# Performance work log

Hardware: AMD Instinct MI355X
Metric: run time of the kernel (lower is better)

The kernel has to match this reference:

```python
import jax, jax.numpy as jnp
import numpy as np

T, N, C, D, S = 512, 32, 1296, 512, 30
NORM_SCALE = 32.0
NEGINF = -1e9


def setup_inputs() -> dict:
    key = jax.random.key(0)
    k1, k2, k3, k4, k5 = jax.random.split(key, 5)
    feats = jax.random.normal(k1, (T * N, D), dtype=jnp.float32)
    classifier_weight = jax.random.normal(k2, (D, C), dtype=jnp.float32)
    labeling = jax.random.randint(k3, (N, S), 1, C)  # targets cannot be blank(0)
    logit_lgts = (T - jax.random.randint(k4, (N,), 0, 32)).astype(jnp.int32)
    labeling_lgts = (S - jax.random.randint(k5, (N,), 0, 5)).astype(jnp.int32)
    return dict(feats=feats, classifier_weight=classifier_weight,
                labeling=labeling, logit_lgts=logit_lgts, labeling_lgts=labeling_lgts)


def _ctc_loss(log_probs, labels, in_lens, lab_lens):
    # log_probs: (T, N, C); labels: (N, S); blank = 0; reduction = 'sum'
    Tt, Nn, Cc = log_probs.shape
    Ss = labels.shape[1]
    L = 2 * Ss + 1
    # extended labeling: blank, l1, blank, l2, ..., blank  -> (N, L)
    ext = jnp.zeros((Nn, L), dtype=labels.dtype).at[:, 1::2].set(labels)
    # gather per-state log-probs: (T, N, L)
    lp_ext = jnp.take_along_axis(log_probs, jnp.broadcast_to(ext[None], (Tt, Nn, L)), axis=2)
    # skip transition s-2 -> s allowed iff s > 1 and ext[s] != ext[s-2]
    skip_ok = jnp.concatenate(
        [jnp.zeros((Nn, 2), dtype=bool), ext[:, 2:] != ext[:, :-2]], axis=1)
    alpha0 = (jnp.full((Nn, L), NEGINF, dtype=log_probs.dtype)
              .at[:, 0].set(lp_ext[0, :, 0])
              .at[:, 1].set(lp_ext[0, :, 1]))

    def step(alpha, inp):
        lp_t, t = inp  # lp_t: (N, L)
        a1 = alpha
        a2 = jnp.pad(alpha[:, :-1], ((0, 0), (1, 0)), constant_values=NEGINF)
        a3 = jnp.where(skip_ok,
                       jnp.pad(alpha[:, :-2], ((0, 0), (2, 0)), constant_values=NEGINF),
                       NEGINF)
        new = jax.nn.logsumexp(jnp.stack([a1, a2, a3], axis=0), axis=0) + lp_t
        # freeze alpha once t reaches a sample's input length
        alpha = jnp.where((t < in_lens)[:, None], new, alpha)
        return alpha, None

    alpha, _ = jax.lax.scan(step, alpha0, (lp_ext[1:], jnp.arange(1, Tt)))
    Ln = 2 * lab_lens + 1  # (N,)
    last = jnp.take_along_axis(alpha, (Ln - 1)[:, None], axis=1)[:, 0]
    last2 = jnp.take_along_axis(alpha, (Ln - 2)[:, None], axis=1)[:, 0]
    nll = -jnp.logaddexp(last, last2)
    return jnp.sum(nll)


def reference(feats, classifier_weight, labeling, logit_lgts, labeling_lgts):
    # RadialCTC: cosine logits with norm_scale, then CTC on log-softmax.
    w_n = classifier_weight / jnp.linalg.norm(classifier_weight, axis=0, keepdims=True)  # (D, C)
    f_n = feats / jnp.linalg.norm(feats, axis=1, keepdims=True)  # (T*N, D)
    logits = NORM_SCALE * (f_n @ w_n)  # (T*N, C)
    log_probs = jax.nn.log_softmax(logits.reshape(T, N, C), axis=-1)
    return _ctc_loss(log_probs, labeling, logit_lgts, labeling_lgts)
```

## Files before the change

### kernel.cpp

```cpp
#include <hip/hip_runtime.h>
#include <stdint.h>
#include <stddef.h>


typedef _Float16 f16;
typedef _Float16 f16x8 __attribute__((ext_vector_type(8)));
typedef float f32x4 __attribute__((ext_vector_type(4)));
typedef __attribute__((address_space(1))) void* as1_void_ptr;
typedef __attribute__((address_space(3))) void* as3_void_ptr;

#define TT 512
#define NN 32
#define CC 1296
#define DD 512
#define SS 30
#define CP 1408
#define LL 61
#define NORM_SCALE 32.0f
#define LOG2E 1.4426950408889634f
#define LN2   0.6931471805599453f

#define PREP_WBLK (CP / 16)
#define PREP_ZBLK 16
#define PREP_FBLK (TT * NN / 4)

#define GEMM_BLK ((TT * NN / 128) * (CP / 128))
#define MEGA_GC  NN
#define MEGA_BLK (MEGA_GC + GEMM_BLK)

__device__ __forceinline__ float fexp2(float x) { return __builtin_amdgcn_exp2f(x); }
__device__ __forceinline__ float flog2(float x) { return __builtin_amdgcn_logf(x); }

__device__ __forceinline__ double dpp_sr1_zero64(double x) {
    long long b = __double_as_longlong(x);
    int lo = (int)(b & 0xFFFFFFFFLL);
    int hi = (int)(b >> 32);
    int lo2 = __builtin_amdgcn_update_dpp(0, lo, 0x138, 0xF, 0xF, false);
    int hi2 = __builtin_amdgcn_update_dpp(0, hi, 0x138, 0xF, 0xF, false);
    return __longlong_as_double(((long long)hi2 << 32) |
                                (unsigned long long)(unsigned int)lo2);
}
__device__ __forceinline__ double dpp_sl1_zero64(double x) {
    long long b = __double_as_longlong(x);
    int lo = (int)(b & 0xFFFFFFFFLL);
    int hi = (int)(b >> 32);
    int lo2 = __builtin_amdgcn_update_dpp(0, lo, 0x130, 0xF, 0xF, false);
    int hi2 = __builtin_amdgcn_update_dpp(0, hi, 0x130, 0xF, 0xF, false);
    return __longlong_as_double(((long long)hi2 << 32) |
                                (unsigned long long)(unsigned int)lo2);
}
__device__ __forceinline__ float dpp_sl1_zero32(float x) {
    int r = __builtin_amdgcn_update_dpp(0, __float_as_int(x), 0x130, 0xF, 0xF, false);
    return __int_as_float(r);
}
template <int CTRL>
__device__ __forceinline__ int dpp_imax_level(int m) {
    int t = __builtin_amdgcn_update_dpp(0, m, CTRL, 0xF, 0xF, false);
    return m > t ? m : t;
}
__device__ __forceinline__ void renorm_d(double& x, int& Mi) {
    int h = (int)(__double_as_longlong(x) >> 32);
    h = dpp_imax_level<0x111>(h);
    h = dpp_imax_level<0x112>(h);
    h = dpp_imax_level<0x114>(h);
    h = dpp_imax_level<0x118>(h);
    int r0 = __builtin_amdgcn_readlane(h, 15);
    int r1 = __builtin_amdgcn_readlane(h, 31);
    int r2 = __builtin_amdgcn_readlane(h, 47);
    int r3 = __builtin_amdgcn_readlane(h, 63);
    int mx = max(max(r0, r1), max(r2, r3));
    int e11 = mx >> 20;
    double scale = __longlong_as_double((long long)(2046 - e11) << 52);
    x *= scale;
    Mi += e11 - 1023;
}

__global__ __launch_bounds__(256) void prep_kernel(const float* __restrict__ W,
                                                   const float* __restrict__ feats,
                                                   f16* __restrict__ wt,
                                                   f16* __restrict__ fn,
                                                   float* __restrict__ sumexp) {
    int bx = blockIdx.x, tid = threadIdx.x;
    if (bx < PREP_WBLK) {
        __shared__ float red[256];
        __shared__ float rqs[16];
        int c0 = bx * 16;
        int cl = tid & 15, dg = tid >> 4;
        int c = c0 + cl;
        float ss = 0.f;
        if (c < CC) {
            for (int d = dg; d < DD; d += 16) {
                float v = W[(size_t)d * CC + c];
                ss += v * v;
            }
        }
        red[tid] = ss;
        __syncthreads();
        if (tid < 16) {
            float s2 = 0.f;
            #pragma unroll
            for (int k = 0; k < 16; ++k) s2 += red[tid + 16 * k];
            rqs[tid] = rsqrtf(s2);
        }
        __syncthreads();
        int c_loc = tid >> 4, dl = tid & 15;
        int cc = c0 + c_loc;
        float rq = rqs[c_loc];
        #pragma unroll 4
        for (int it = 0; it < 32; ++it) {
            int d = dl + it * 16;
            float v = (cc < CC) ? W[(size_t)d * CC + cc] * rq : 0.f;
            wt[(size_t)cc * DD + d] = (f16)v;
        }
    } else if (bx < PREP_WBLK + PREP_ZBLK) {
        int zb = bx - PREP_WBLK;
        float4 z = {0.f, 0.f, 0.f, 0.f};
        ((float4*)sumexp)[zb * 256 + tid] = z;
    } else {
        int fb = bx - PREP_WBLK - PREP_ZBLK;
        int wv = (fb * 256 + tid) >> 6;
        int lane = tid & 63;
        const float4* src = (const float4*)(feats + (size_t)wv * DD) + lane * 2;
        float4 a = src[0], b = src[1];
        float ss = a.x*a.x + a.y*a.y + a.z*a.z + a.w*a.w
                 + b.x*b.x + b.y*b.y + b.z*b.z + b.w*b.w;
        #pragma unroll
        for (int off = 32; off; off >>= 1) ss += __shfl_xor(ss, off);
        float r = rsqrtf(ss);
        f16x8 o;
        o[0]=(f16)(a.x*r); o[1]=(f16)(a.y*r); o[2]=(f16)(a.z*r); o[3]=(f16)(a.w*r);
        o[4]=(f16)(b.x*r); o[5]=(f16)(b.y*r); o[6]=(f16)(b.z*r); o[7]=(f16)(b.w*r);
        *(f16x8*)(fn + (size_t)wv * DD + lane * 8) = o;
    }
}

template <int NT>
__device__ __forceinline__ void gather_chunk(const f16* __restrict__ pb0,
                                             const f16* __restrict__ pb1,
                                             const f16* __restrict__ A,
                                             float* __restrict__ lp_lab,
                                             int n, int c, int rbase, int lane) {
    int lm = lane & 15, hi = lane >> 4;
    const f16* pa0 = A + ((size_t)(c * 128 + rbase + lm) * NN + n) * DD + hi * 8;
    f32x4 acc[NT][2];
    #pragma unroll
    for (int i = 0; i < NT; ++i) {
        acc[i][0] = (f32x4){0.f, 0.f, 0.f, 0.f};
        acc[i][1] = (f32x4){0.f, 0.f, 0.f, 0.f};
    }
    for (int kb = 0; kb < 16; ++kb) {
        f16x8 bf0 = *(const f16x8*)(pb0 + kb * 32);
        f16x8 bf1 = *(const f16x8*)(pb1 + kb * 32);
        #pragma unroll
        for (int i = 0; i < NT; ++i) {
            f16x8 af = *(const f16x8*)(pa0 + (size_t)(i * 16) * NN * DD + kb * 32);
            acc[i][0] = __builtin_amdgcn_mfma_f32_16x16x32_f16(af, bf0, acc[i][0], 0, 0, 0);
            acc[i][1] = __builtin_amdgcn_mfma_f32_16x16x32_f16(af, bf1, acc[i][1], 0, 0, 0);
        }
    }
    #pragma unroll
    for (int i = 0; i < NT; ++i) {
        #pragma unroll
        for (int jn = 0; jn < 2; ++jn) {
            int jc = jn * 16 + lm;
            if (jc >= 31) continue;
            float4 o;
            o.x = acc[i][jn][0] * (NORM_SCALE * LOG2E);
            o.y = acc[i][jn][1] * (NORM_SCALE * LOG2E);
            o.z = acc[i][jn][2] * (NORM_SCALE * LOG2E);
            o.w = acc[i][jn][3] * (NORM_SCALE * LOG2E);
            *(float4*)&lp_lab[((size_t)n * 31 + jc) * TT
                              + c * 128 + rbase + i * 16 + hi * 4] = o;
        }
    }
}

__global__ __launch_bounds__(256) void mega_kernel(const f16* __restrict__ A,
                                                   const f16* __restrict__ B,
                                                   const int* __restrict__ labels,
                                                   const int* __restrict__ in_lens,
                                                   const int* __restrict__ lab_lens,
                                                   float* __restrict__ sumexp,
                                                   float* __restrict__ lp_lab,
                                                   double* __restrict__ part) {
    __shared__ __align__(16) f16 sm[8192];
    int bx = blockIdx.x;
    int tid = threadIdx.x;
    int w = tid >> 6, lane = tid & 63;
    int lm = lane & 15, hi = lane >> 4;
    int sw = (lm >> 1) & 3;

    if (bx >= MEGA_GC) {
        int j = bx - MEGA_GC;
        int x = j & 7, rr = j >> 3;
        int bm = x * 16 + (rr & 15);
        int bn = rr >> 4;
        int wm = w >> 1, wn = w & 1;
        f32x4 acc[4][4];
        f32x4 zero = {0.f, 0.f, 0.f, 0.f};
        #pragma unroll
        for (int i = 0; i < 4; ++i)
            #pragma unroll
            for (int jj = 0; jj < 4; ++jj) acc[i][jj] = zero;

        for (int kb = 0; kb < 16; ++kb) {
            #pragma unroll
            for (int p = 0; p < 2; ++p) {
                int s = p * 256 + tid;
                int row = s >> 2;
                int ch = (s & 3) ^ ((row >> 1) & 3);
                const f16* ga = A + (size_t)(bm * 128 + row) * DD + kb * 32 + ch * 8;
                const f16* gb = B + (size_t)(bn * 128 + row) * DD + kb * 32 + ch * 8;
                __builtin_amdgcn_global_load_lds((as1_void_ptr)ga,
                    (as3_void_ptr)&sm[(p * 256 + w * 64) * 8], 16, 0, 0);
                __builtin_amdgcn_global_load_lds((as1_void_ptr)gb,
                    (as3_void_ptr)&sm[4096 + (p * 256 + w * 64) * 8], 16, 0, 0);
            }
            __syncthreads();
            f16x8 af[4], bf[4];
            #pragma unroll
            for (int i = 0; i < 4; ++i)
                af[i] = *(const f16x8*)&sm[(wm * 64 + i * 16 + lm) * 32 + (hi ^ sw) * 8];
            #pragma unroll
            for (int jj = 0; jj < 4; ++jj)
                bf[jj] = *(const f16x8*)&sm[4096 + (wn * 64 + jj * 16 + lm) * 32 + (hi ^ sw) * 8];
            #pragma unroll
            for (int i = 0; i < 4; ++i)
                #pragma unroll
                for (int jj = 0; jj < 4; ++jj)
                    acc[i][jj] = __builtin_amdgcn_mfma_f32_16x16x32_f16(af[i], bf[jj], acc[i][jj], 0, 0, 0);
            __syncthreads();
        }
        #pragma unroll
        for (int i = 0; i < 4; ++i) {
            float rs[4] = {0.f, 0.f, 0.f, 0.f};
            #pragma unroll
            for (int jj = 0; jj < 4; ++jj) {
                int c = bn * 128 + wn * 64 + jj * 16 + lm;
                bool ok = (c < CC);
                #pragma unroll
                for (int r = 0; r < 4; ++r)
                    rs[r] += ok ? fexp2(acc[i][jj][r] * (NORM_SCALE * LOG2E)) : 0.f;
            }
            #pragma unroll
            for (int off = 1; off < 16; off <<= 1) {
                #pragma unroll
                for (int r = 0; r < 4; ++r) rs[r] += __shfl_xor(rs[r], off);
            }
            if (lm == 0) {
                int rowb = bm * 128 + wm * 64 + i * 16 + hi * 4;
                #pragma unroll
                for (int r = 0; r < 4; ++r) atomicAdd(&sumexp[rowb + r], rs[r]);
            }
        }
        return;
    }

    int n = bx;
    if (w >= 2) {
        __builtin_amdgcn_s_setprio(2);
        int cls0 = (lm == 0) ? 0 : labels[n * SS + lm - 1];
        int cls1 = (lm >= 15) ? 0 : labels[n * SS + lm + 15];
        const f16* pb0 = B + (size_t)cls0 * DD + hi * 8;
        const f16* pb1 = B + (size_t)cls1 * DD + hi * 8;
        int cA = (w == 2) ? 0 : 3;
        int cB = (w == 2) ? 1 : 2;
        gather_chunk<4>(pb0, pb1, A, lp_lab, n, cA, 0, lane);
        gather_chunk<4>(pb0, pb1, A, lp_lab, n, cA, 64, lane);
        __syncthreads();
        gather_chunk<4>(pb0, pb1, A, lp_lab, n, cB, 0, lane);
        gather_chunk<4>(pb0, pb1, A, lp_lab, n, cB, 64, lane);
        __builtin_amdgcn_s_setprio(0);
        __syncthreads();
        __syncthreads();
        return;
    }

    int s = lane;
    bool valid = s < LL;
    int ext = (valid && (s & 1)) ? labels[n * SS + (s >> 1)] : 0;
    int jmap = (valid && (s & 1)) ? ((s >> 1) + 1) : 0;
    int Tin = in_lens[n];
    const float* lpr = lp_lab + ((size_t)n * 31 + jmap) * TT;
    double* vb = (double*)sm;

    if (w == 0) {
        int ext2 = __shfl_up(ext, 2);
        double skipd = ((s >= 2) && valid && (ext != ext2)) ? 1.0 : 0.0;
        double sk1 = dpp_sr1_zero64(skipd);
        double sk2 = dpp_sr1_zero64(sk1);
        double kk2 = skipd * sk2;
        const float4* g4 = (const float4*)lpr;
        double beta = 0.0;
        int Mif = 0;

        auto stepL = [&](float lp) {
            double P = (double)fexp2(lp);
            double b1 = dpp_sr1_zero64(beta);
            double b2 = dpp_sr1_zero64(b1);
            beta = (beta + b1 + b2 * skipd) * P;
        };
        auto step2 = [&](float lp1, float lp2) {
            double q  = (double)fexp2(lp1);
            double P2 = (double)fexp2(lp2);
            double q1 = dpp_sr1_zero64(q);
            double q2 = dpp_sr1_zero64(q1);
            double c1 = q + q1;
            double c2 = fma(skipd, q + q2, q1);
            double c3 = fma(sk1, q1, skipd * q2);
            double c4 = kk2 * q2;
            double b1 = dpp_sr1_zero64(beta);
            double b2 = dpp_sr1_zero64(b1);
            double b3 = dpp_sr1_zero64(b2);
            double b4 = dpp_sr1_zero64(b3);
            double u = fma(c1, b1, q * beta);
            double v2 = fma(c3, b3, c2 * b2);
            beta = (u + fma(c4, b4, v2)) * P2;
        };

        __builtin_amdgcn_s_setprio(3);
        __syncthreads();
        float4 q0 = g4[0];
        beta = (s <= 1) ? (double)fexp2(q0.x) : 0.0;
        stepL(q0.y); stepL(q0.z); stepL(q0.w);
        renorm_d(beta, Mif);
        float4 cu = g4[1];
        for (int gi = 1; gi <= 31; ++gi) {
            float4 nx = g4[gi < 31 ? gi + 1 : 31];
            step2(cu.x, cu.y); step2(cu.z, cu.w);
            if (gi & 1) renorm_d(beta, Mif);
            cu = nx;
        }
        __syncthreads();
        cu = g4[32];
        for (int gi = 32; gi <= 63; ++gi) {
            float4 nx = g4[gi < 63 ? gi + 1 : 63];
            step2(cu.x, cu.y); step2(cu.z, cu.w);
            if (gi & 1) renorm_d(beta, Mif);
            cu = nx;
        }
        renorm_d(beta, Mif);
        __syncthreads();
        __builtin_amdgcn_s_setprio(0);
        double pr = beta * vb[s];
        #pragma unroll
        for (int off = 32; off; off >>= 1) pr += __shfl_xor(pr, off);
        if (s == 0) {
            long long bb = __double_as_longlong(pr);
            int e = (int)(bb >> 52) - 1023;
            double mant = __longlong_as_double((bb & 0xFFFFFFFFFFFFFLL) | (1023LL << 52));
            part[n] = (double)flog2((float)mant) + (double)(e + Mif) + vb[64];
        }
        return;
    }

    {
        float maskf = valid ? 1.f : 0.f;
        int extd1 = __shfl_down(ext, 1);
        int extd2 = __shfl_down(ext, 2);
        int extd3 = __shfl_down(ext, 3);
        int extd4 = __shfl_down(ext, 4);
        double k2d = ((s + 2) < LL && extd2 != ext)   ? 1.0 : 0.0;
        double k3d = ((s + 3) < LL && extd3 != extd1) ? 1.0 : 0.0;
        double k4d = ((s + 4) < LL && extd4 != extd2) ? 1.0 : 0.0;
        int Ln = 2 * lab_lens[n] + 1;
        double v = (s == Ln - 1 || s == Ln - 2) ? 1.0 : 0.0;
        int Mib = 0;

        auto step2b = [&](float lph, float lpl) {
            float p  = maskf * fexp2(lph);
            float rr = maskf * fexp2(lpl);
            float p1 = dpp_sl1_zero32(p);
            float p2 = dpp_sl1_zero32(p1);
            float p3 = dpp_sl1_zero32(p2);
            float p4 = dpp_sl1_zero32(p3);
            float r1 = dpp_sl1_zero32(rr);
            float r2 = dpp_sl1_zero32(r1);
            double rd = (double)rr, rd1 = (double)r1, rd2 = (double)r2;
            double c0 = (double)p * rd;
            double c1 = (double)p1 * (rd + rd1);
            double c2 = (double)p2 * fma(k2d, rd + rd2, rd1);
            double c3 = (double)p3 * fma(k3d, rd1, k2d * rd2);
            double c4 = (double)p4 * (k2d * rd2) * k4d;
            double v1 = dpp_sl1_zero64(v);
            double v2 = dpp_sl1_zero64(v1);
            double v3 = dpp_sl1_zero64(v2);
            double v4 = dpp_sl1_zero64(v3);
            double u  = fma(c1, v1, c0 * v);
            double t2 = fma(c3, v3, c2 * v2);
            v = u + fma(c4, v4, t2);
        };
        auto step1b = [&](float lph) {
            float p = maskf * fexp2(lph);
            double u  = (double)p * v;
            double u1 = dpp_sl1_zero64(u);
            double u2 = dpp_sl1_zero64(u1);
            v = u + u1 + k2d * u2;
        };

        __builtin_amdgcn_s_setprio(3);
        __syncthreads();
        int tc = Tin - 1;
        float h0 = lpr[tc], l0 = lpr[tc - 1];
        int rnc = 0;
        while (tc >= 385) {
            int tn = tc - 2;
            float h1 = (tn >= 384) ? lpr[tn] : 0.f;
            float l1 = (tn >= 385) ? lpr[tn - 1] : 0.f;
            step2b(h0, l0);
            if (((++rnc) & 3) == 0) renorm_d(v, Mib);
            tc = tn; h0 = h1; l0 = l1;
        }
        if (tc == 384) { step1b(h0); tc = 383; }
        renorm_d(v, Mib);
        __syncthreads();
        tc = 383;
        h0 = lpr[tc]; l0 = lpr[tc - 1];
        rnc = 0;
        while (tc >= 257) {
            int tn = tc - 2;
            float h1 = (tn >= 257) ? lpr[tn] : 0.f;
            float l1 = (tn >= 257) ? lpr[tn - 1] : 0.f;
            step2b(h0, l0);
            if (((++rnc) & 3) == 0) renorm_d(v, Mib);
            tc = tn; h0 = h1; l0 = l1;
        }
        renorm_d(v, Mib);
        vb[s] = v;
        if (s == 0) vb[64] = (double)Mib;
        __builtin_amdgcn_s_setprio(0);
        __syncthreads();
        return;
    }
}

__global__ __launch_bounds__(1024) void final_kernel(const float* __restrict__ sumexp,
                                                     const int* __restrict__ in_lens,
                                                     const double* __restrict__ part,
                                                     float* __restrict__ out) {
    int tid = threadIdx.x;
    int v = tid >> 6, lane = tid & 63;
    __shared__ float nl[NN];
    #pragma unroll
    for (int k = 0; k < 2; ++k) {
        int n = v * 2 + k;
        int Tin = in_lens[n];
        double ms = 0.0;
        for (int t = lane; t < Tin; t += 64)
            ms += (double)flog2(sumexp[(size_t)t * NN + n]);
        #pragma unroll
        for (int off = 32; off; off >>= 1) ms += __shfl_xor(ms, off);
        if (lane == 0) nl[n] = (float)(-(part[n] - ms) * LN2);
    }
    __syncthreads();
    if (tid == 0) {
        float t = 0.f;
        for (int i = 0; i < NN; ++i) t += nl[i];
        out[0] = t;
    }
}

extern "C" void kernel_launch(void* const* d_in, const int* in_sizes, int n_in,
                              void* d_out, int out_size, void* d_ws, size_t ws_size,
                              hipStream_t stream) {
    const float* feats        = (const float*)d_in[0];
    const float* W            = (const float*)d_in[1];
    const int*   labeling     = (const int*)d_in[2];
    const int*   logit_lgts   = (const int*)d_in[3];
    const int*   labeling_lgts= (const int*)d_in[4];
    float* out = (float*)d_out;
    char* ws = (char*)d_ws;

    size_t off = 0;
    f16*   wt     = (f16*)(ws + off);   off += (size_t)CP * DD * 2;
    f16*   fn     = (f16*)(ws + off);   off += (size_t)TT * NN * DD * 2;
    float* sumexp = (float*)(ws + off); off += (size_t)TT * NN * 4;
    float* lp_lab = (float*)(ws + off); off += (size_t)NN * 31 * TT * 4;
    double* part  = (double*)(ws + off); off += NN * 8;

    prep_kernel<<<PREP_WBLK + PREP_ZBLK + PREP_FBLK, 256, 0, stream>>>(
        W, feats, wt, fn, sumexp);
    mega_kernel<<<MEGA_BLK, 256, 0, stream>>>(fn, wt, labeling, logit_lgts,
                                              labeling_lgts, sumexp, lp_lab, part);
    final_kernel<<<1, 1024, 0, stream>>>(sumexp, logit_lgts, part, out);

    (void)in_sizes; (void)n_in; (void)out_size; (void)ws_size;
}
```

Measured before the change: 168.5 us.

## Replace two-step fused beta recursion with single-step loop and fewer renorms

The backward (beta) CTC recursion drops the fused two-timestep update, which used extra DPP shifts and precomputed coefficients, and goes back to a plain one-timestep step. Renormalisation now runs every 8 steps instead of every 4 fused steps. The gather warps are rewritten as a loop over a packed chunk order with a per-warp row base. The loop boundaries change (384/256 instead of 385/257), so the aim is a shorter dependency chain per step in exchange for twice as many serial steps, with possible boundary or overflow risks.

```diff
diff --git a/kernel.cpp b/kernel.cpp
--- a/kernel.cpp
+++ b/kernel.cpp
@@ -48,10 +48,6 @@
     int hi2 = __builtin_amdgcn_update_dpp(0, hi, 0x130, 0xF, 0xF, false);
     return __longlong_as_double(((long long)hi2 << 32) |
                                 (unsigned long long)(unsigned int)lo2);
-}
-__device__ __forceinline__ float dpp_sl1_zero32(float x) {
-    int r = __builtin_amdgcn_update_dpp(0, __float_as_int(x), 0x130, 0xF, 0xF, false);
-    return __int_as_float(r);
 }
 template <int CTRL>
 __device__ __forceinline__ int dpp_imax_level(int m) {
@@ -259,17 +255,17 @@
     int n = bx;
     if (w >= 2) {
         __builtin_amdgcn_s_setprio(2);
+        int rbase = (w - 2) * 64;
         int cls0 = (lm == 0) ? 0 : labels[n * SS + lm - 1];
         int cls1 = (lm >= 15) ? 0 : labels[n * SS + lm + 15];
         const f16* pb0 = B + (size_t)cls0 * DD + hi * 8;
         const f16* pb1 = B + (size_t)cls1 * DD + hi * 8;
-        int cA = (w == 2) ? 0 : 3;
-        int cB = (w == 2) ? 1 : 2;
-        gather_chunk<4>(pb0, pb1, A, lp_lab, n, cA, 0, lane);
-        gather_chunk<4>(pb0, pb1, A, lp_lab, n, cA, 64, lane);
-        __syncthreads();
-        gather_chunk<4>(pb0, pb1, A, lp_lab, n, cB, 0, lane);
-        gather_chunk<4>(pb0, pb1, A, lp_lab, n, cB, 64, lane);
+        #pragma unroll 1
+        for (int ci = 0; ci < 4; ++ci) {
+            int c = (0x2130 >> (ci * 4)) & 3;
+            gather_chunk<4>(pb0, pb1, A, lp_lab, n, c, rbase, lane);
+            if (ci == 1) __syncthreads();
+        }
         __builtin_amdgcn_s_setprio(0);
         __syncthreads();
         __syncthreads();
@@ -356,74 +352,35 @@
 
     {
         float maskf = valid ? 1.f : 0.f;
-        int extd1 = __shfl_down(ext, 1);
         int extd2 = __shfl_down(ext, 2);
-        int extd3 = __shfl_down(ext, 3);
-        int extd4 = __shfl_down(ext, 4);
-        double k2d = ((s + 2) < LL && extd2 != ext)   ? 1.0 : 0.0;
-        double k3d = ((s + 3) < LL && extd3 != extd1) ? 1.0 : 0.0;
-        double k4d = ((s + 4) < LL && extd4 != extd2) ? 1.0 : 0.0;
+        double k2d = ((s + 2) < LL && extd2 != ext) ? 1.0 : 0.0;
         int Ln = 2 * lab_lens[n] + 1;
         double v = (s == Ln - 1 || s == Ln - 2) ? 1.0 : 0.0;
         int Mib = 0;
 
-        auto step2b = [&](float lph, float lpl) {
-            float p  = maskf * fexp2(lph);
-            float rr = maskf * fexp2(lpl);
-            float p1 = dpp_sl1_zero32(p);
-            float p2 = dpp_sl1_zero32(p1);
-            float p3 = dpp_sl1_zero32(p2);
-            float p4 = dpp_sl1_zero32(p3);
-            float r1 = dpp_sl1_zero32(rr);
-            float r2 = dpp_sl1_zero32(r1);
-            double rd = (double)rr, rd1 = (double)r1, rd2 = (double)r2;
-            double c0 = (double)p * rd;
-            double c1 = (double)p1 * (rd + rd1);
-            double c2 = (double)p2 * fma(k2d, rd + rd2, rd1);
-            double c3 = (double)p3 * fma(k3d, rd1, k2d * rd2);
-            double c4 = (double)p4 * (k2d * rd2) * k4d;
-            double v1 = dpp_sl1_zero64(v);
-            double v2 = dpp_sl1_zero64(v1);
-            double v3 = dpp_sl1_zero64(v2);
-            double v4 = dpp_sl1_zero64(v3);
-            double u  = fma(c1, v1, c0 * v);
-            double t2 = fma(c3, v3, c2 * v2);
-            v = u + fma(c4, v4, t2);
-        };
         auto step1b = [&](float lph) {
             float p = maskf * fexp2(lph);
             double u  = (double)p * v;
             double u1 = dpp_sl1_zero64(u);
             double u2 = dpp_sl1_zero64(u1);
-            v = u + u1 + k2d * u2;
+            v = fma(k2d, u2, u + u1);
         };
 
         __builtin_amdgcn_s_setprio(3);
         __syncthreads();
         int tc = Tin - 1;
-        float h0 = lpr[tc], l0 = lpr[tc - 1];
         int rnc = 0;
-        while (tc >= 385) {
-            int tn = tc - 2;
-            float h1 = (tn >= 384) ? lpr[tn] : 0.f;
-            float l1 = (tn >= 385) ? lpr[tn - 1] : 0.f;
-            step2b(h0, l0);
-            if (((++rnc) & 3) == 0) renorm_d(v, Mib);
-            tc = tn; h0 = h1; l0 = l1;
-        }
-        if (tc == 384) { step1b(h0); tc = 383; }
+        while (tc >= 384) {
+            step1b(lpr[tc]);
+            if (((++rnc) & 7) == 0) renorm_d(v, Mib);
+            --tc;
+        }
         renorm_d(v, Mib);
         __syncthreads();
-        tc = 383;
-        h0 = lpr[tc]; l0 = lpr[tc - 1];
-        rnc = 0;
-        while (tc >= 257) {
-            int tn = tc - 2;
-            float h1 = (tn >= 257) ? lpr[tn] : 0.f;
-            float l1 = (tn >= 257) ? lpr[tn - 1] : 0.f;
-            step2b(h0, l0);
-            if (((++rnc) & 3) == 0) renorm_d(v, Mib);
-            tc = tn; h0 = h1; l0 = l1;
+        while (tc >= 256) {
+            step1b(lpr[tc]);
+            if (((++rnc) & 7) == 0) renorm_d(v, Mib);
+            --tc;
         }
         renorm_d(v, Mib);
         vb[s] = v;
```

New measurement: 180.2 us. 1.07x slower.
